# Performance work log

Measured on AMD Instinct MI355X. Metric: run time of the kernel, lower is better.

The kernel has to match this reference:

```python
import jax, jax.numpy as jnp
import numpy as np

T = 40           # rollout steps
ATT_TEMP = 5.0   # Arbiter attention temperature
ACT_CLIP = 3.5


def setup_inputs() -> dict:
    key = jax.random.key(0)
    ks = jax.random.split(key, 6)
    B, D = 262144, 128
    # states: vel >= 0, dx > 0 (dx is a divisor)
    unscaled_s = jax.random.uniform(ks[0], (B, T, 7), dtype=jnp.float32)
    unscaled_s = unscaled_s.at[:, :, 0].set(unscaled_s[:, :, 0] * 20.0 + 5.0)   # vel
    unscaled_s = unscaled_s.at[:, :, 2].set(unscaled_s[:, :, 2] * 4.0 - 2.0)    # dv (leader)
    unscaled_s = unscaled_s.at[:, :, 3].set(unscaled_s[:, :, 3] * 50.0 + 10.0)  # dx (leader)
    unscaled_s = unscaled_s.at[:, :, 5].set(unscaled_s[:, :, 5] * 4.0 - 2.0)    # dv (merger)
    unscaled_s = unscaled_s.at[:, :, 6].set(unscaled_s[:, :, 6] * 50.0 + 10.0)  # dx (merger)
    # idm params: all strictly positive (sqrt + division)
    p = jax.random.uniform(ks[1], (B, 5), dtype=jnp.float32)
    idm_param = jnp.stack([
        p[:, 0] * 10.0 + 20.0,  # desired_v
        p[:, 1] * 1.0 + 0.5,    # desired_tgap
        p[:, 2] * 3.0 + 1.0,    # min_jamx
        p[:, 3] * 2.0 + 0.5,    # max_act
        p[:, 4] * 2.0 + 0.5,    # min_act
    ], axis=1)
    decoder_output = jax.random.normal(ks[2], (B, D), dtype=jnp.float32)
    W1 = jax.random.normal(ks[3], (D, 100), dtype=jnp.float32) * 0.05
    b1 = jnp.zeros((100,), dtype=jnp.float32)
    W2 = jax.random.normal(ks[4], (100, T), dtype=jnp.float32) * 0.05
    b2 = jnp.zeros((T,), dtype=jnp.float32)
    return {"unscaled_s": unscaled_s, "idm_param": idm_param,
            "decoder_output": decoder_output, "W1": W1, "b1": b1, "W2": W2, "b2": b2}


def _idm_driver(vel, dv, dx, idm_param):
    # vel/dv/dx: [B, T, 1]; idm_param: [B, 5]
    p = idm_param[:, None, :]  # [B, 1, 5]
    desired_v, desired_tgap, min_jamx, max_act, min_act = (
        p[..., 0:1], p[..., 1:2], p[..., 2:3], p[..., 3:4], p[..., 4:5])
    desired_gap = min_jamx + desired_tgap * vel + vel * dv / (2.0 * jnp.sqrt(max_act * min_act))
    act = max_act * (1.0 - (vel / desired_v) ** 4 - (desired_gap / dx) ** 2)
    return jnp.clip(act, -ACT_CLIP, ACT_CLIP)


def reference(unscaled_s, idm_param, decoder_output, W1, b1, W2, b2):
    B = unscaled_s.shape[0]
    # The 40-step loop has no cross-step dependency -> fully vectorized over T.
    s = unscaled_s[:, :T, :]                 # [B, T, 7]
    vel = s[:, :, 0:1]
    fl_seq = _idm_driver(vel, s[:, :, 2:3], s[:, :, 3:4], idm_param)  # [B, T, 1]
    fm_seq = _idm_driver(vel, s[:, :, 5:6], s[:, :, 6:7], idm_param)  # [B, T, 1]
    # Arbiter: two dense layers + temperature sigmoid
    h = decoder_output @ W1 + b1
    logits = h @ W2 + b2                      # [B, T]
    att_scores = jax.nn.sigmoid(ATT_TEMP * logits).reshape(B, T, 1)
    act_seq = att_scores * fl_seq + (1.0 - att_scores) * fm_seq
    return act_seq, att_scores
```

## Files before the change

kernel.cpp:

```cpp
#include <hip/hip_runtime.h>


#define TT 40
#define DD 128
#define ACT_CLIP 3.5f
#define ATT_TEMP 5.0f

typedef short short8 __attribute__((ext_vector_type(8)));
typedef float f32x4 __attribute__((ext_vector_type(4)));

__device__ __forceinline__ unsigned int bf16_rne(float v) {
    unsigned int u = __float_as_uint(v);
    return (u + 0x7FFFu + ((u >> 16) & 1u)) >> 16;
}

__global__ __launch_bounds__(256) void precompute_pack(
    const float* __restrict__ W1, const float* __restrict__ b1,
    const float* __restrict__ W2, const float* __restrict__ b2,
    unsigned int* __restrict__ wpack,
    float* __restrict__ bcp)
{
    int idx = blockIdx.x * 256 + threadIdx.x;
    if (idx < 1536) {
        int l   = idx & 63;
        int rec = idx >> 6;
        int h   = rec & 1;
        int sn  = rec >> 1;
        int n   = sn % 3, s = sn / 3;
        int col = n * 16 + (l & 15);
        int k0  = s * 32 + (l >> 4) * 8;
        unsigned short hv[8];
#pragma unroll
        for (int j = 0; j < 8; ++j) {
            float v = 0.0f;
            if (col < TT) {
                int k = k0 + j;
                for (int m = 0; m < 100; ++m)
                    v = fmaf(W1[k * 100 + m], W2[m * TT + col], v);
            }
            unsigned int hi = bf16_rne(v);
            float hif = __uint_as_float(hi << 16);
            unsigned int lo = bf16_rne(v - hif);
            hv[j] = (unsigned short)(h == 0 ? hi : lo);
        }
        uint4 o;
        o.x = hv[0] | ((unsigned)hv[1] << 16);
        o.y = hv[2] | ((unsigned)hv[3] << 16);
        o.z = hv[4] | ((unsigned)hv[5] << 16);
        o.w = hv[6] | ((unsigned)hv[7] << 16);
        reinterpret_cast<uint4*>(wpack)[idx] = o;
    } else if (idx < 1536 + 48) {
        int t = idx - 1536;
        float v = 0.0f;
        if (t < TT) {
            v = b2[t];
            for (int m = 0; m < 100; ++m)
                v = fmaf(b1[m], W2[m * TT + t], v);
        }
        bcp[t] = v;
    }
}

__global__ __launch_bounds__(256, 4) void matvec_att(
    const float* __restrict__ x,
    const unsigned int* __restrict__ wpack,
    const float* __restrict__ bcp,
    float* __restrict__ attout)
{
    __shared__ unsigned int swp[6144];
    __shared__ float sbc[48];
    __shared__ float satt[64 * TT];

    int tid = threadIdx.x;
    {
        const uint4* src = reinterpret_cast<const uint4*>(wpack);
        uint4* dst = reinterpret_cast<uint4*>(swp);
#pragma unroll
        for (int i = 0; i < 6; ++i) dst[tid + 256 * i] = src[tid + 256 * i];
        if (tid < 48) sbc[tid] = bcp[tid];
    }
    __syncthreads();

    int wave = tid >> 6, lane = tid & 63;
    int l15 = lane & 15, lk = lane >> 4;
    size_t blk = blockIdx.x;
    size_t row0 = blk * 64 + wave * 16 + l15;
    const float* xr = x + row0 * DD;

    float4 xv[8];
#pragma unroll
    for (int s = 0; s < 4; ++s) {
        xv[2 * s]     = *reinterpret_cast<const float4*>(xr + s * 32 + lk * 8);
        xv[2 * s + 1] = *reinterpret_cast<const float4*>(xr + s * 32 + lk * 8 + 4);
    }

    f32x4 acc[3] = {f32x4{0,0,0,0}, f32x4{0,0,0,0}, f32x4{0,0,0,0}};

#pragma unroll
    for (int s = 0; s < 4; ++s) {
        float fs[8] = {xv[2*s].x, xv[2*s].y, xv[2*s].z, xv[2*s].w,
                       xv[2*s+1].x, xv[2*s+1].y, xv[2*s+1].z, xv[2*s+1].w};
        union { unsigned int u[4]; short8 v; } ah, al;
#pragma unroll
        for (int p = 0; p < 4; ++p) {
            unsigned int u0 = __float_as_uint(fs[2*p]);
            unsigned int u1 = __float_as_uint(fs[2*p+1]);
            ah.u[p] = (u0 >> 16) | (u1 & 0xFFFF0000u);
            float r0 = fs[2*p]   - __uint_as_float(u0 & 0xFFFF0000u);
            float r1 = fs[2*p+1] - __uint_as_float(u1 & 0xFFFF0000u);
            al.u[p] = (__float_as_uint(r0) >> 16) |
                      (__float_as_uint(r1) & 0xFFFF0000u);
        }
#pragma unroll
        for (int n = 0; n < 3; ++n) {
            int base = (s * 3 + n) * 512;
            short8 bh = *reinterpret_cast<const short8*>(&swp[base + lane * 4]);
            short8 bl = *reinterpret_cast<const short8*>(&swp[base + 256 + lane * 4]);
            acc[n] = __builtin_amdgcn_mfma_f32_16x16x32_bf16(ah.v, bh, acc[n], 0, 0, 0);
            acc[n] = __builtin_amdgcn_mfma_f32_16x16x32_bf16(al.v, bh, acc[n], 0, 0, 0);
            acc[n] = __builtin_amdgcn_mfma_f32_16x16x32_bf16(ah.v, bl, acc[n], 0, 0, 0);
        }
    }

#pragma unroll
    for (int n = 0; n < 3; ++n) {
        int col = n * 16 + l15;
        if (col < TT) {
            float bias = sbc[col];
#pragma unroll
            for (int r = 0; r < 4; ++r) {
                int rowl = wave * 16 + lk * 4 + r;
                float L = acc[n][r] + bias;
                satt[rowl * TT + col] =
                    __builtin_amdgcn_rcpf(1.0f + __expf(-ATT_TEMP * L));
            }
        }
    }
    __syncthreads();

    float4* dst = reinterpret_cast<float4*>(attout + blk * 64 * TT);
    const float4* s4 = reinterpret_cast<const float4*>(satt);
    dst[tid]       = s4[tid];
    dst[tid + 256] = s4[tid + 256];
    if (tid < 128) dst[tid + 512] = s4[tid + 512];
}

__global__ __launch_bounds__(320) void epilogue_k(
    const float* __restrict__ us, const float* __restrict__ prm,
    const float* __restrict__ attg,
    float* __restrict__ act)
{
    __shared__ float sus[320 * 31];

    int tid = threadIdx.x;
    size_t blk = blockIdx.x;

    f32x4 a4 = reinterpret_cast<const f32x4*>(attg)[blk * 320u + tid];

    const f32x4* su = reinterpret_cast<const f32x4*>(us) + blk * 2240u;
#pragma unroll
    for (int i = 0; i < 7; ++i) {
        unsigned f = (unsigned)tid + 320u * i;
        f32x4 v = __builtin_nontemporal_load(su + f);
        unsigned item = f / 7u;
        unsigned slot = f - item * 7u;
        float* w = &sus[item * 31u + slot * 4u];
        w[0] = v.x; w[1] = v.y; w[2] = v.z; w[3] = v.w;
    }

    unsigned int row_g = (unsigned)(blk * 320u + tid) / 10u;
    const float* pr = prm + (size_t)row_g * 5u;
    float desired_v    = pr[0];
    float desired_tgap = pr[1];
    float min_jamx     = pr[2];
    float max_act      = pr[3];
    float min_act      = pr[4];

    __syncthreads();

    float inv_dv = __builtin_amdgcn_rcpf(desired_v);
    float coef   = 0.5f / sqrtf(max_act * min_act);

    const float* fp = &sus[(unsigned)tid * 31u];
    float ares[4];
#pragma unroll
    for (int tt = 0; tt < 4; ++tt) {
        float vel = fp[tt * 7 + 0];
        float dvl = fp[tt * 7 + 2], dxl = fp[tt * 7 + 3];
        float dvm = fp[tt * 7 + 5], dxm = fp[tt * 7 + 6];

        float r  = vel * inv_dv;
        float r2 = r * r;
        float common = 1.0f - r2 * r2;
        float base = fmaf(desired_tgap, vel, min_jamx);
        float gl = fmaf(vel * dvl, coef, base);
        float gm = fmaf(vel * dvm, coef, base);
        float ql = gl * __builtin_amdgcn_rcpf(dxl);
        float qm = gm * __builtin_amdgcn_rcpf(dxm);
        float al = max_act * (common - ql * ql);
        float am = max_act * (common - qm * qm);
        al = fminf(fmaxf(al, -ACT_CLIP), ACT_CLIP);
        am = fminf(fmaxf(am, -ACT_CLIP), ACT_CLIP);
        float a = (tt == 0) ? a4.x : (tt == 1) ? a4.y : (tt == 2) ? a4.z : a4.w;
        ares[tt] = fmaf(a, al - am, am);
    }
    f32x4 res = {ares[0], ares[1], ares[2], ares[3]};
    __builtin_nontemporal_store(res, reinterpret_cast<f32x4*>(act) + blk * 320u + tid);
}

extern "C" void kernel_launch(void* const* d_in, const int* in_sizes, int n_in,
                              void* d_out, int out_size, void* d_ws, size_t ws_size,
                              hipStream_t stream) {
    const float* us  = (const float*)d_in[0];
    const float* prm = (const float*)d_in[1];
    const float* x   = (const float*)d_in[2];
    const float* W1  = (const float*)d_in[3];
    const float* b1  = (const float*)d_in[4];
    const float* W2  = (const float*)d_in[5];
    const float* b2  = (const float*)d_in[6];
    float* out = (float*)d_out;

    int B = in_sizes[1] / 5;

    unsigned int* wpack = (unsigned int*)d_ws;
    float* bcp = (float*)((char*)d_ws + 24576);

    float* attout = out + (size_t)B * TT;

    hipLaunchKernelGGL(precompute_pack, dim3(7), dim3(256), 0, stream,
                       W1, b1, W2, b2, wpack, bcp);
    hipLaunchKernelGGL(matvec_att, dim3(B / 64), dim3(256), 0, stream,
                       x, wpack, bcp, attout);
    hipLaunchKernelGGL(epilogue_k, dim3(B / 32), dim3(320), 0, stream,
                       us, prm, attout, out);
}
```

Before: 114.3 us.

## Software-pipeline epilogue over four chunks per block with double-buffered register loads

The epilogue kernel now processes four 32-row chunks per block, launching a quarter as many blocks. Global loads for the next chunk are issued into a second register buffer while the current chunk is computed from shared memory, so memory latency overlaps with compute. The cost is more registers per thread (two sets of seven float4 plus attention vectors), which may lower occupancy, and extra barriers per block.

```diff
diff --git a/kernel.cpp b/kernel.cpp
--- a/kernel.cpp
+++ b/kernel.cpp
@@ -145,67 +145,95 @@
     if (tid < 128) dst[tid + 512] = s4[tid + 512];
 }
 
-__global__ __launch_bounds__(320) void epilogue_k(
+__global__ __launch_bounds__(320) void epilogue_pipe(
     const float* __restrict__ us, const float* __restrict__ prm,
     const float* __restrict__ attg,
-    float* __restrict__ act)
+    float* __restrict__ act,
+    int nb)
 {
     __shared__ float sus[320 * 31];
 
-    int tid = threadIdx.x;
-    size_t blk = blockIdx.x;
-
-    f32x4 a4 = reinterpret_cast<const f32x4*>(attg)[blk * 320u + tid];
-
-    const f32x4* su = reinterpret_cast<const f32x4*>(us) + blk * 2240u;
-#pragma unroll
-    for (int i = 0; i < 7; ++i) {
-        unsigned f = (unsigned)tid + 320u * i;
-        f32x4 v = __builtin_nontemporal_load(su + f);
-        unsigned item = f / 7u;
-        unsigned slot = f - item * 7u;
-        float* w = &sus[item * 31u + slot * 4u];
-        w[0] = v.x; w[1] = v.y; w[2] = v.z; w[3] = v.w;
-    }
-
-    unsigned int row_g = (unsigned)(blk * 320u + tid) / 10u;
-    const float* pr = prm + (size_t)row_g * 5u;
-    float desired_v    = pr[0];
-    float desired_tgap = pr[1];
-    float min_jamx     = pr[2];
-    float max_act      = pr[3];
-    float min_act      = pr[4];
-
-    __syncthreads();
-
-    float inv_dv = __builtin_amdgcn_rcpf(desired_v);
-    float coef   = 0.5f / sqrtf(max_act * min_act);
-
-    const float* fp = &sus[(unsigned)tid * 31u];
-    float ares[4];
-#pragma unroll
-    for (int tt = 0; tt < 4; ++tt) {
-        float vel = fp[tt * 7 + 0];
-        float dvl = fp[tt * 7 + 2], dxl = fp[tt * 7 + 3];
-        float dvm = fp[tt * 7 + 5], dxm = fp[tt * 7 + 6];
-
-        float r  = vel * inv_dv;
-        float r2 = r * r;
-        float common = 1.0f - r2 * r2;
-        float base = fmaf(desired_tgap, vel, min_jamx);
-        float gl = fmaf(vel * dvl, coef, base);
-        float gm = fmaf(vel * dvm, coef, base);
-        float ql = gl * __builtin_amdgcn_rcpf(dxl);
-        float qm = gm * __builtin_amdgcn_rcpf(dxm);
-        float al = max_act * (common - ql * ql);
-        float am = max_act * (common - qm * qm);
-        al = fminf(fmaxf(al, -ACT_CLIP), ACT_CLIP);
-        am = fminf(fmaxf(am, -ACT_CLIP), ACT_CLIP);
-        float a = (tt == 0) ? a4.x : (tt == 1) ? a4.y : (tt == 2) ? a4.z : a4.w;
-        ares[tt] = fmaf(a, al - am, am);
-    }
-    f32x4 res = {ares[0], ares[1], ares[2], ares[3]};
-    __builtin_nontemporal_store(res, reinterpret_cast<f32x4*>(act) + blk * 320u + tid);
+    const int tid = threadIdx.x;
+    const unsigned blk = blockIdx.x;
+    const unsigned nbu = (unsigned)nb;
+
+    f32x4 rvA[7], rvB[7], aA, aB;
+
+    auto issue = [&](unsigned cid, f32x4* rv, f32x4& a4) {
+        const f32x4* su = reinterpret_cast<const f32x4*>(us) + (size_t)cid * 2240u;
+#pragma unroll
+        for (int i = 0; i < 7; ++i)
+            rv[i] = __builtin_nontemporal_load(su + tid + 320 * i);
+        a4 = reinterpret_cast<const f32x4*>(attg)[(size_t)cid * 320u + tid];
+    };
+    auto writeL = [&](const f32x4* rv) {
+#pragma unroll
+        for (int i = 0; i < 7; ++i) {
+            unsigned f = (unsigned)tid + 320u * i;
+            unsigned item = f / 7u;
+            unsigned slot = f - item * 7u;
+            float* w = &sus[item * 31u + slot * 4u];
+            w[0] = rv[i].x; w[1] = rv[i].y; w[2] = rv[i].z; w[3] = rv[i].w;
+        }
+    };
+    auto consume = [&](unsigned cid, f32x4 a4) {
+        unsigned row_g = cid * 32u + (unsigned)tid / 10u;
+        const float* pr = prm + (size_t)row_g * 5u;
+        float desired_v    = pr[0];
+        float desired_tgap = pr[1];
+        float min_jamx     = pr[2];
+        float max_act      = pr[3];
+        float min_act      = pr[4];
+        float inv_dv = __builtin_amdgcn_rcpf(desired_v);
+        float coef   = 0.5f / sqrtf(max_act * min_act);
+
+        const float* fp = &sus[(unsigned)tid * 31u];
+        float ares[4];
+#pragma unroll
+        for (int tt = 0; tt < 4; ++tt) {
+            float vel = fp[tt * 7 + 0];
+            float dvl = fp[tt * 7 + 2], dxl = fp[tt * 7 + 3];
+            float dvm = fp[tt * 7 + 5], dxm = fp[tt * 7 + 6];
+
+            float r  = vel * inv_dv;
+            float r2 = r * r;
+            float common = 1.0f - r2 * r2;
+            float base = fmaf(desired_tgap, vel, min_jamx);
+            float gl = fmaf(vel * dvl, coef, base);
+            float gm = fmaf(vel * dvm, coef, base);
+            float ql = gl * __builtin_amdgcn_rcpf(dxl);
+            float qm = gm * __builtin_amdgcn_rcpf(dxm);
+            float al = max_act * (common - ql * ql);
+            float am = max_act * (common - qm * qm);
+            al = fminf(fmaxf(al, -ACT_CLIP), ACT_CLIP);
+            am = fminf(fmaxf(am, -ACT_CLIP), ACT_CLIP);
+            float a = (tt==0) ? a4.x : (tt==1) ? a4.y : (tt==2) ? a4.z : a4.w;
+            ares[tt] = fmaf(a, al - am, am);
+        }
+        f32x4 res = {ares[0], ares[1], ares[2], ares[3]};
+        __builtin_nontemporal_store(res,
+            reinterpret_cast<f32x4*>(act) + (size_t)cid * 320u + tid);
+    };
+
+    issue(blk, rvA, aA);
+    writeL(rvA);
+    issue(blk + nbu, rvB, aB);
+    __syncthreads();
+    consume(blk, aA);
+    __syncthreads();
+    writeL(rvB);
+    issue(blk + 2u * nbu, rvA, aA);
+    __syncthreads();
+    consume(blk + nbu, aB);
+    __syncthreads();
+    writeL(rvA);
+    issue(blk + 3u * nbu, rvB, aB);
+    __syncthreads();
+    consume(blk + 2u * nbu, aA);
+    __syncthreads();
+    writeL(rvB);
+    __syncthreads();
+    consume(blk + 3u * nbu, aB);
 }
 
 extern "C" void kernel_launch(void* const* d_in, const int* in_sizes, int n_in,
@@ -231,6 +259,7 @@
                        W1, b1, W2, b2, wpack, bcp);
     hipLaunchKernelGGL(matvec_att, dim3(B / 64), dim3(256), 0, stream,
                        x, wpack, bcp, attout);
-    hipLaunchKernelGGL(epilogue_k, dim3(B / 32), dim3(320), 0, stream,
-                       us, prm, attout, out);
-}
+    int nb = B / 32 / 4;
+    hipLaunchKernelGGL(epilogue_pipe, dim3(nb), dim3(320), 0, stream,
+                       us, prm, attout, out, nb);
+}
```

New measurement: 121.0 us. 5.9% more time.
